# Kernel tuning notes

Measured on AMD Instinct MI355X. Metric: run time of the kernel, lower is better.

The kernel has to match this reference:

```python
import jax, jax.numpy as jnp
import numpy as np

INV_SQRT_2 = float(1.0 / np.sqrt(2.0))
INV_SQRT_3 = float(1.0 / np.sqrt(3.0))


def _silu(x):
    return x * jax.nn.sigmoid(x)


def _residual_stack(x, Ws):
    # Ws: (n_layers, 2, d, d); each layer: two (Dense -> silu), residual add, *1/sqrt(2)
    for l in range(Ws.shape[0]):
        y = x
        for i in range(Ws.shape[1]):
            y = _silu(y @ Ws[l, i])
        x = (x + y) * INV_SQRT_2
    return x


def _eff_bilinear(basis, m, id_reduce, ragged, W, n_edges, kmax):
    # basis: (T, B), m: (T, I), W: (I, B, O). Ragged rows packed into dense (E, Kmax, .)
    b2 = jnp.zeros((n_edges, kmax, basis.shape[1]), basis.dtype).at[id_reduce, ragged].set(basis)
    m2 = jnp.zeros((n_edges, kmax, m.shape[1]), m.dtype).at[id_reduce, ragged].set(m)
    sum_k = jnp.einsum('ekb,eki->ebi', b2, m2)          # (E, B, I)
    return jnp.einsum('ebi,ibo->eo', sum_k, W)          # (E, O)


def setup_inputs() -> dict:
    key = jax.random.key(0)
    N, E, K = 8000, 80000, 6
    T = E * K
    D, DR, DC, DS, DT3, DB, DQ = 128, 16, 16, 16, 64, 64, 64
    ks = jax.random.split(key, 32)
    r = lambda i, shape, s=1.0: jax.random.normal(ks[i], shape, jnp.float32) * s
    w = 0.05
    return dict(
        h=r(0, (N, D)), m_st=r(1, (E, D)),
        rbf_h=jax.random.uniform(ks[2], (E, DR)),
        rbf3=jax.random.uniform(ks[3], (E, DR)),
        cbf3=jax.random.uniform(ks[4], (T, DC)),
        sbf4=jax.random.uniform(ks[5], (T, DS)),
        idx_s=jax.random.randint(ks[6], (E,), 0, N),
        idx_t=jax.random.randint(ks[7], (E,), 0, N),
        idx_swap=jax.random.permutation(ks[8], E),
        id3_kt=jax.random.randint(ks[9], (T,), 0, E),
        id3_st=jnp.repeat(jnp.arange(E), K),
        id3_ragged_idx=jnp.tile(jnp.arange(K), E),
        edge_nb_idx=jnp.repeat(jnp.arange(E), K),
        edge_nb_ragged_idx=jnp.tile(jnp.arange(K), E),
        Kt=K, Kq=K,
        W_skip=r(10, (D, D), w),
        Wt_mkt=r(11, (D, D), w), Wt_rbf=r(12, (DR, D), w), Wt_down=r(13, (D, DT3), w),
        Wt_cbf=r(14, (DT3, DC, DB), w), Wt_up_st=r(15, (DB, D), w), Wt_up_ts=r(16, (DB, D), w),
        Wq_down=r(17, (D, DQ), w), Wq_sbf=r(18, (DQ, DS, DQ), w),
        Wq_up_st=r(19, (DQ, D), w), Wq_up_ts=r(20, (DQ, D), w),
        Wres_before=r(21, (1, 2, D, D), w), Wres_after=r(22, (2, 2, D, D), w),
        Wres_m=r(23, (1, 2, D, D), w),
        W_ae_rbf=r(24, (DR, D), w), W_ae_dense=r(25, (D, D), w), W_ae_res=r(26, (2, 2, D, D), w),
        W_asi=r(27, (3 * D, D), w),
    )


def reference(h, m_st, rbf_h, rbf3, cbf3, sbf4, idx_s, idx_t, idx_swap, id3_kt,
              id3_st, id3_ragged_idx, edge_nb_idx, edge_nb_ragged_idx, Kt, Kq,
              W_skip, Wt_mkt, Wt_rbf, Wt_down, Wt_cbf, Wt_up_st, Wt_up_ts,
              Wq_down, Wq_sbf, Wq_up_st, Wq_up_ts, Wres_before, Wres_after,
              Wres_m, W_ae_rbf, W_ae_dense, W_ae_res, W_asi):
    N, E = h.shape[0], m_st.shape[0]

    x_skip = m_st @ W_skip

    # Quadruplet interaction (ScaleFactor == identity)
    m_d = _silu(m_st @ Wq_down)                       # (E, emb_quad)
    m_nb = m_d[edge_nb_idx]                            # (E_NB, emb_quad)
    xq = _eff_bilinear(sbf4, m_nb, edge_nb_idx, edge_nb_ragged_idx, Wq_sbf, E, Kq)
    x4 = (_silu(xq @ Wq_up_st) + _silu(xq @ Wq_up_ts)[idx_swap]) * INV_SQRT_2

    # Triplet interaction
    m_kt = _silu(m_st @ Wt_mkt)
    m_kt = m_kt * (rbf3 @ Wt_rbf)                      # scale_rbf identity
    m_kt = _silu(m_kt @ Wt_down)                       # (E, emb_triplet)
    m_kt = m_kt[id3_kt]                                # (T, emb_triplet)
    xt = _eff_bilinear(cbf3, m_kt, id3_st, id3_ragged_idx, Wt_cbf, E, Kt)
    x3 = (_silu(xt @ Wt_up_st) + _silu(xt @ Wt_up_ts)[idx_swap]) * INV_SQRT_2

    x = (x_skip + x3 + x4) * INV_SQRT_3
    x = _residual_stack(x, Wres_before)
    m = (m_st + x) * INV_SQRT_2
    m = _residual_stack(m, Wres_after)

    # AtomEmbedding: rbf-gated scatter-add of edge messages to target atoms
    x_ae = m * (rbf_h @ W_ae_rbf)
    h2 = jax.ops.segment_sum(x_ae, idx_t, num_segments=N)   # scale_sum identity
    h2 = _silu(h2 @ W_ae_dense)
    h2 = _residual_stack(h2, W_ae_res)
    h_new = (h + h2) * INV_SQRT_2

    # AtomSelfInteraction
    m2 = _silu(jnp.concatenate([h_new[idx_s], h_new[idx_t], m], axis=-1) @ W_asi)
    m2 = _residual_stack(m2, Wres_m)
    m_out = (m + m2) * INV_SQRT_2
    return h_new, m_out
```

## Files before the change

kernel.cpp:

```cpp
#include <hip/hip_runtime.h>

#define INV_SQRT_2 0.70710678118654752440f
#define INV_SQRT_3 0.57735026918962576451f

typedef __bf16 bf16_t;
typedef __bf16 bf16x8 __attribute__((ext_vector_type(8)));
typedef __bf16 bf16x4 __attribute__((ext_vector_type(4)));
typedef float f32x4 __attribute__((ext_vector_type(4)));

__device__ __forceinline__ float toF(float x) { return x; }
__device__ __forceinline__ float toF(bf16_t x) { return (float)x; }
__device__ __forceinline__ float siluf(float x) { return x / (1.f + __expf(-x)); }

__device__ __forceinline__ bf16x8 ld8(const bf16_t* p) { return *(const bf16x8*)p; }
__device__ __forceinline__ bf16x8 ld8(const float* p) {
  bf16x8 r;
#pragma unroll
  for (int j = 0; j < 8; ++j) r[j] = (bf16_t)p[j];
  return r;
}

__device__ __forceinline__ float ldsc(const void* p, int f32, size_t i) {
  return f32 ? ((const float*)p)[i] : toF(((const bf16_t*)p)[i]);
}

__device__ __forceinline__ f32x4 MFMA(bf16x8 a, bf16x8 b, f32x4 c) {
  return __builtin_amdgcn_mfma_f32_16x16x32_bf16(a, b, c, 0, 0, 0);
}

__device__ __forceinline__ void zero8(f32x4 (&a)[8]) {
#pragma unroll
  for (int i = 0; i < 8; ++i)
#pragma unroll
    for (int q = 0; q < 4; ++q) a[i][q] = 0.f;
}
__device__ __forceinline__ void zero4(f32x4 (&a)[4]) {
#pragma unroll
  for (int i = 0; i < 4; ++i)
#pragma unroll
    for (int q = 0; q < 4; ++q) a[i][q] = 0.f;
}

__device__ __forceinline__ bf16x8 ldB(const bf16_t* Bp, int ks, int nt, int NT, int lane) {
  return *(const bf16x8*)(Bp + ((((size_t)ks * NT + nt) * 64 + lane) << 3));
}

__device__ __forceinline__ void ldA(bf16x8 (&af)[4], const void* p, int f32, size_t row, int g) {
  if (f32) {
    const float* q = (const float*)p + row * 128 + (g << 3);
#pragma unroll
    for (int ks = 0; ks < 4; ++ks) af[ks] = ld8(q + ks * 32);
  } else {
    const bf16_t* q = (const bf16_t*)p + row * 128 + (g << 3);
#pragma unroll
    for (int ks = 0; ks < 4; ++ks) af[ks] = ld8(q + ks * 32);
  }
}

struct St8 { bf16x8 v[8]; };
__device__ __forceinline__ void issue8(St8& r, const bf16_t* src, int tid) {
#pragma unroll
  for (int i = 0; i < 8; ++i) r.v[i] = *(const bf16x8*)(src + ((i * 256 + tid) << 3));
}
__device__ __forceinline__ void commit8(const St8& r, bf16_t* dst, int tid) {
#pragma unroll
  for (int i = 0; i < 8; ++i) *(bf16x8*)&dst[(i * 256 + tid) << 3] = r.v[i];
}
struct St4 { bf16x8 v[4]; };
__device__ __forceinline__ void issue4(St4& r, const bf16_t* src, int tid) {
#pragma unroll
  for (int i = 0; i < 4; ++i) r.v[i] = *(const bf16x8*)(src + ((i * 256 + tid) << 3));
}
__device__ __forceinline__ void commit4(const St4& r, bf16_t* dst, int tid) {
#pragma unroll
  for (int i = 0; i < 4; ++i) *(bf16x8*)&dst[(i * 256 + tid) << 3] = r.v[i];
}

template <int KS, int NT>
__device__ __forceinline__ void pass_glob(f32x4 (&acc)[NT], const bf16x8* af,
                                          const bf16_t* Wbuf, int lane) {
#pragma unroll
  for (int ks = 0; ks < KS; ++ks)
#pragma unroll
    for (int nt = 0; nt < NT; ++nt)
      acc[nt] = MFMA(af[ks], *(const bf16x8*)&Wbuf[((ks * NT + nt) * 64 + lane) << 3], acc[nt]);
}
template <int KS>
__device__ __forceinline__ void pass_slab(f32x4 (&acc)[8], const bf16_t* slab,
                                          const bf16_t* Wbuf, int lane) {
  const int rc = lane & 15, g = lane >> 4;
#pragma unroll
  for (int ks = 0; ks < KS; ++ks) {
    bf16x8 a = *(const bf16x8*)&slab[rc * 136 + ks * 32 + (g << 3)];
#pragma unroll
    for (int nt = 0; nt < 8; ++nt)
      acc[nt] = MFMA(a, *(const bf16x8*)&Wbuf[((ks * 8 + nt) * 64 + lane) << 3], acc[nt]);
  }
}

__global__ void k_detect(const unsigned short* __restrict__ probe, int* __restrict__ flag) {
  __shared__ int cnt;
  if (threadIdx.x == 0) cnt = 0;
  __syncthreads();
  int bad = 0;
  for (int i = threadIdx.x; i < 256; i += 64) {
    unsigned int u = (unsigned int)probe[i] << 16;
    float v = __uint_as_float(u);
    if (!(v == v) || fabsf(v) > 4.f || v < -0.25f) bad++;
  }
  atomicAdd(&cnt, bad);
  __syncthreads();
  if (threadIdx.x == 0) *flag = (cnt > 16) ? 1 : 0;
}

__global__ void k_zero(float* __restrict__ p, int n) {
  int i = blockIdx.x * blockDim.x + threadIdx.x;
  if (i < n) p[i] = 0.f;
}

struct RDesc { const void* src; int K, N, Kpad, dstoff, mode; };
struct RTable { RDesc d[25]; };

__global__ void k_repack(const int* __restrict__ flag, RTable tab, bf16_t* __restrict__ out) {
  const int ws = *flag;
  RDesc d = tab.d[blockIdx.y];
  int p = blockIdx.x * 256 + threadIdx.x;
  int sz = d.Kpad * d.N;
  if (p >= sz) return;
  const int bilin = d.mode & 1;
  const int Koff = d.mode >> 1;
  int NT = d.N >> 4;
  int j = p & 7;
  int lane = (p >> 3) & 63;
  int q = p >> 9;
  int nt = q % NT, ks = q / NT;
  int k = ks * 32 + ((lane >> 4) << 3) + j;
  int col = nt * 16 + (lane & 15);
  size_t si = bilin ? ((size_t)(k & 63) * 16 + (k >> 6)) * 64 + col
                    : (size_t)(k + Koff) * d.N + col;
  float v = (k < d.K) ? ldsc(d.src, ws, si) : 0.f;
  bf16_t hi = (bf16_t)v;
  out[d.dstoff + p] = hi;
  out[d.dstoff + sz + p] = (bf16_t)(v - (float)hi);
}

__global__ __launch_bounds__(256) void k_bil(const int* __restrict__ flag,
    const void* __restrict__ basis, const bf16_t* __restrict__ msrc,
    const int* __restrict__ gidx, const bf16_t* __restrict__ Wc,
    bf16_t* __restrict__ out) {
  const int ws = *flag;
  __shared__ __align__(16) bf16_t Ms[96 * 72];
  __shared__ __align__(16) float Bas[16 * 100];
  __shared__ __align__(16) bf16_t P[16384];
  const int tid = threadIdx.x;
  const int e0 = blockIdx.x * 16;
#pragma unroll
  for (int it = 0; it < 3; ++it) {
    int c = tid + it * 256;
    int j = c >> 3, part = c & 7;
    int row = gidx[e0 * 6 + j];
    *(bf16x8*)&Ms[j * 72 + part * 8] = ld8(msrc + (size_t)row * 64 + part * 8);
  }
#pragma unroll
  for (int it = 0; it < 6; ++it) {
    int c = tid + it * 256;
    Bas[(c / 96) * 100 + (c % 96)] = ldsc(basis, ws, (size_t)e0 * 96 + c);
  }
  __syncthreads();
  {
    const int e = tid >> 4, sub = tid & 15, i0 = sub * 4;
    float acc[16][4];
#pragma unroll
    for (int b = 0; b < 16; ++b)
#pragma unroll
      for (int j = 0; j < 4; ++j) acc[b][j] = 0.f;
#pragma unroll
    for (int k = 0; k < 6; ++k) {
      bf16x4 mv = *(const bf16x4*)&Ms[(e * 6 + k) * 72 + i0];
      float mf[4];
#pragma unroll
      for (int j = 0; j < 4; ++j) mf[j] = (float)mv[j];
      const float* bp = &Bas[e * 100 + k * 16];
#pragma unroll
      for (int b4 = 0; b4 < 4; ++b4) {
        f32x4 bv = *(const f32x4*)&bp[b4 * 4];
#pragma unroll
        for (int bb = 0; bb < 4; ++bb)
#pragma unroll
          for (int j = 0; j < 4; ++j) acc[b4 * 4 + bb][j] += bv[bb] * mf[j];
      }
    }
#pragma unroll
    for (int b = 0; b < 16; ++b) {
      int kk = b * 64 + i0;
      int ks = kk >> 5, r5 = kk & 31;
      int lane_hi = r5 >> 3, jj = r5 & 7;
      bf16x4 w;
#pragma unroll
      for (int j = 0; j < 4; ++j) w[j] = (bf16_t)acc[b][j];
      *(bf16x4*)&P[ks * 512 + lane_hi * 128 + e * 8 + jj] = w;
    }
  }
  __syncthreads();
  const int lane = tid & 63, wid = tid >> 6;
  const int rc = lane & 15, g = lane >> 4;
  f32x4 oa[4];
  zero4(oa);
  if (ws) {
#pragma unroll
    for (int k4 = 0; k4 < 8; ++k4)
#pragma unroll
      for (int j = 0; j < 4; ++j) {
        int ks = k4 * 4 + j;
        bf16x8 a = *(const bf16x8*)&P[ks * 512 + lane * 8];
        oa[j] = MFMA(a, ldB(Wc, ks, wid, 4, lane), oa[j]);
        oa[j] = MFMA(a, ldB(Wc + 65536, ks, wid, 4, lane), oa[j]);
      }
  } else {
#pragma unroll
    for (int k4 = 0; k4 < 8; ++k4)
#pragma unroll
      for (int j = 0; j < 4; ++j) {
        int ks = k4 * 4 + j;
        bf16x8 a = *(const bf16x8*)&P[ks * 512 + lane * 8];
        oa[j] = MFMA(a, ldB(Wc, ks, wid, 4, lane), oa[j]);
      }
  }
  f32x4 oacc = (oa[0] + oa[1]) + (oa[2] + oa[3]);
  bf16_t* op = out + ((size_t)e0 + g * 4) * 64 + wid * 16 + rc;
#pragma unroll
  for (int r = 0; r < 4; ++r) op[(size_t)r * 64] = (bf16_t)oacc[r];
}

__global__ __launch_bounds__(256, 2) void k_mkt2(const int* __restrict__ flag,
    const void* __restrict__ mst, const void* __restrict__ rbf3,
    const bf16_t* __restrict__ Wm, const bf16_t* __restrict__ Wr,
    bf16_t* __restrict__ out) {
  const int ws = *flag;
  __shared__ __align__(16) bf16_t Wb[2][16384];
  __shared__ __align__(16) bf16_t Wrl[8192];
  const int tid = threadIdx.x;
  const int lane = tid & 63, wid = tid >> 6;
  const int grow0 = blockIdx.x * 64 + wid * 16;
  const int rc = lane & 15, g = lane >> 4;
  St8 s8;
  issue8(s8, Wm, tid);
  bf16x8 wr[4];
#pragma unroll
  for (int i = 0; i < 4; ++i) wr[i] = *(const bf16x8*)(Wr + ((i * 256 + tid) << 3));
  commit8(s8, Wb[0], tid);
#pragma unroll
  for (int i = 0; i < 4; ++i) *(bf16x8*)&Wrl[(i * 256 + tid) << 3] = wr[i];
  __syncthreads();
  bf16x8 af[4];
  ldA(af, mst, ws, (size_t)(grow0 + rc), g);
  bf16x8 az;
#pragma unroll
  for (int j = 0; j < 8; ++j) az[j] = (bf16_t)0.f;
  if (g < 2) {
    if (ws) az = ld8((const float*)rbf3 + (size_t)(grow0 + rc) * 16 + (g << 3));
    else    az = ld8((const bf16_t*)rbf3 + (size_t)(grow0 + rc) * 16 + (g << 3));
  }
  f32x4 ag[8];
  zero8(ag);
#pragma unroll
  for (int nt = 0; nt < 8; ++nt) {
    ag[nt] = MFMA(az, *(const bf16x8*)&Wrl[(nt * 64 + lane) << 3], ag[nt]);
    if (ws) ag[nt] = MFMA(az, *(const bf16x8*)&Wrl[4096 + ((nt * 64 + lane) << 3)], ag[nt]);
  }
  f32x4 am[8];
  zero8(am);
  if (ws) issue8(s8, Wm + 16384, tid);
  pass_glob<4, 8>(am, af, Wb[0], lane);
  if (ws) {
    commit8(s8, Wb[1], tid);
    __syncthreads();
    pass_glob<4, 8>(am, af, Wb[1], lane);
  }
  bf16_t* op = out + (size_t)(grow0 + g * 4) * 128 + rc;
#pragma unroll
  for (int nt = 0; nt < 8; ++nt)
#pragma unroll
    for (int r = 0; r < 4; ++r)
      op[(size_t)r * 128 + nt * 16] = (bf16_t)(siluf(am[nt][r]) * ag[nt][r]);
}

__global__ __launch_bounds__(256, 4) void k_gemmE2(const int* __restrict__ flag, int a_rt,
    const void* __restrict__ A, const bf16_t* __restrict__ W, bf16_t* __restrict__ out) {
  const int ws = *flag;
  const int af32 = a_rt & ws;
  __shared__ __align__(16) bf16_t Wb[2][8192];
  const int tid = threadIdx.x;
  const int lane = tid & 63, wid = tid >> 6;
  const int grow0 = blockIdx.x * 64 + wid * 16;
  const int rc = lane & 15, g = lane >> 4;
  St4 s4;
  issue4(s4, W, tid);
  commit4(s4, Wb[0], tid);
  __syncthreads();
  bf16x8 af[4];
  ldA(af, A, af32, (size_t)(grow0 + rc), g);
  f32x4 acc[4];
  zero4(acc);
  if (ws) issue4(s4, W + 8192, tid);
  pass_glob<4, 4>(acc, af, Wb[0], lane);
  if (ws) {
    commit4(s4, Wb[1], tid);
    __syncthreads();
    pass_glob<4, 4>(acc, af, Wb[1], lane);
  }
  bf16_t* op = out + (size_t)(grow0 + g * 4) * 64 + rc;
#pragma unroll
  for (int nt = 0; nt < 4; ++nt)
#pragma unroll
    for (int r = 0; r < 4; ++r) op[(size_t)r * 64 + nt * 16] = (bf16_t)siluf(acc[nt][r]);
}

__global__ __launch_bounds__(256, 2) void k_gemmN2(const int* __restrict__ flag,
    const float* __restrict__ A, const bf16_t* __restrict__ W, bf16_t* __restrict__ out) {
  const int ws = *flag;
  __shared__ __align__(16) bf16_t Wb[2][16384];
  const int tid = threadIdx.x;
  const int lane = tid & 63, wid = tid >> 6;
  const int grow0 = blockIdx.x * 64 + wid * 16;
  const int rc = lane & 15, g = lane >> 4;
  St8 s8;
  issue8(s8, W, tid);
  commit8(s8, Wb[0], tid);
  __syncthreads();
  bf16x8 af[4];
  {
    const float* q = A + (size_t)(grow0 + rc) * 128 + (g << 3);
#pragma unroll
    for (int ks = 0; ks < 4; ++ks) af[ks] = ld8(q + ks * 32);
  }
  f32x4 acc[8];
  zero8(acc);
  if (ws) issue8(s8, W + 16384, tid);
  pass_glob<4, 8>(acc, af, Wb[0], lane);
  if (ws) {
    commit8(s8, Wb[1], tid);
    __syncthreads();
    pass_glob<4, 8>(acc, af, Wb[1], lane);
  }
  bf16_t* op = out + (size_t)(grow0 + g * 4) * 128 + rc;
#pragma unroll
  for (int nt = 0; nt < 8; ++nt)
#pragma unroll
    for (int r = 0; r < 4; ++r) op[(size_t)r * 128 + nt * 16] = (bf16_t)siluf(acc[nt][r]);
}

__global__ __launch_bounds__(256, 2) void k_comb2(const int* __restrict__ flag,
    const void* __restrict__ mst, const bf16_t* __restrict__ xt,
    const bf16_t* __restrict__ xq, const int* __restrict__ idx_swap,
    const bf16_t* Wsk, const bf16_t* Wtst, const bf16_t* Wtts,
    const bf16_t* Wqst, const bf16_t* Wqts, bf16_t* __restrict__ X) {
  const int ws = *flag;
  __shared__ __align__(16) bf16_t Wb[2][16384];
  const int tid = threadIdx.x;
  const int lane = tid & 63, wid = tid >> 6;
  const int grow0 = blockIdx.x * 64 + wid * 16;
  const int rc = lane & 15, g = lane >> 4;
  const int arow = grow0 + rc;
  const int srow = idx_swap[arow];
  const bf16_t* wseq[5] = {Wsk, Wtst, Wtts, Wqst, Wqts};
  const int SZs[5] = {16384, 8192, 8192, 8192, 8192};
  St8 s8;
  issue8(s8, wseq[0], tid);
  commit8(s8, Wb[0], tid);
  __syncthreads();
  int cur = 0;
  const int NP = ws ? 2 : 1;
  f32x4 total[8], acc[8];
  zero8(acc);
  bf16x8 af[4];
  for (int l = 0; l < 5; ++l) {
    if (l == 0) {
      ldA(af, mst, ws, (size_t)arow, g);
    } else {
      const bf16_t* asrc = (l <= 2) ? xt : xq;
      int r = (l == 1 || l == 3) ? arow : srow;
      af[0] = ld8(asrc + (size_t)r * 64 + (g << 3));
      af[1] = ld8(asrc + (size_t)r * 64 + 32 + (g << 3));
    }
    for (int p = 0; p < NP; ++p) {
      const bool last = (l == 4) && (p == NP - 1);
      if (!last) issue8(s8, (ws && p == 0) ? wseq[l] + SZs[l] : wseq[l + 1], tid);
      if (l == 0) pass_glob<4, 8>(acc, af, Wb[cur], lane);
      else        pass_glob<2, 8>(acc, af, Wb[cur], lane);
      if (!last) {
        commit8(s8, Wb[cur ^ 1], tid);
        __syncthreads();
        cur ^= 1;
      }
    }
    if (l == 0) {
#pragma unroll
      for (int nt = 0; nt < 8; ++nt) total[nt] = acc[nt] * INV_SQRT_3;
    } else {
#pragma unroll
      for (int nt = 0; nt < 8; ++nt)
#pragma unroll
        for (int r = 0; r < 4; ++r)
          total[nt][r] += siluf(acc[nt][r]) * (INV_SQRT_2 * INV_SQRT_3);
    }
    zero8(acc);
  }
  bf16_t* op = X + (size_t)(grow0 + g * 4) * 128 + rc;
#pragma unroll
  for (int nt = 0; nt < 8; ++nt)
#pragma unroll
    for (int r = 0; r < 4; ++r) op[(size_t)r * 128 + nt * 16] = (bf16_t)total[nt][r];
}

__global__ __launch_bounds__(256, 2) void k_resE2(const int* __restrict__ flag,
    const bf16_t* __restrict__ Xg, const void* __restrict__ mst,
    const bf16_t* W0, const bf16_t* W1, const bf16_t* W2,
    const bf16_t* W3, const bf16_t* W4, const bf16_t* W5,
    bf16_t* __restrict__ outg) {
  const int ws = *flag;
  __shared__ __align__(16) bf16_t Xs[64 * 136];
  __shared__ __align__(16) bf16_t Ys[64 * 136];
  __shared__ __align__(16) bf16_t Wb[16384];
  const int tid = threadIdx.x;
  const int lane = tid & 63, wid = tid >> 6;
  const int grow0 = blockIdx.x * 64 + wid * 16;
  const int rc = lane & 15, g = lane >> 4;
  bf16_t* slabX = Xs + wid * (16 * 136);
  bf16_t* slabY = Ys + wid * (16 * 136);
  const bf16_t* Wl[6] = {W0, W1, W2, W3, W4, W5};
  const bf16_t* seq[12];
  int NW;
  if (ws) {
    NW = 12;
#pragma unroll
    for (int l = 0; l < 6; ++l) { seq[2 * l] = Wl[l]; seq[2 * l + 1] = Wl[l] + 16384; }
  } else {
    NW = 6;
#pragma unroll
    for (int l = 0; l < 6; ++l) seq[l] = Wl[l];
  }
  St8 s8;
  issue8(s8, seq[0], tid);
#pragma unroll
  for (int i = 0; i < 4; ++i) {
    int o = (i * 64 + lane) * 8, r = o >> 7, c = o & 127;
    *(bf16x8*)&slabX[r * 136 + c] = *(const bf16x8*)&Xg[(size_t)(grow0 + r) * 128 + c];
  }
  commit8(s8, Wb, tid);
  __syncthreads();
  f32x4 acc[8];
  zero8(acc);
  for (int s = 0; s < NW; ++s) {
    if (s + 1 < NW) issue8(s8, seq[s + 1], tid);
    const int gg = ws ? (s >> 1) : s;
    const int fin = ws ? (s & 1) : 1;
    pass_slab<4>(acc, (gg & 1) ? slabY : slabX, Wb, lane);
    __syncthreads();
    if (s + 1 < NW) commit8(s8, Wb, tid);
    if (fin) {
      if ((gg & 1) == 0) {
#pragma unroll
        for (int nt = 0; nt < 8; ++nt)
#pragma unroll
          for (int r = 0; r < 4; ++r)
            slabY[(g * 4 + r) * 136 + nt * 16 + rc] = (bf16_t)siluf(acc[nt][r]);
      } else {
#pragma unroll
        for (int nt = 0; nt < 8; ++nt)
#pragma unroll
          for (int r = 0; r < 4; ++r) {
            int ix = (g * 4 + r) * 136 + nt * 16 + rc;
            float v = ((float)slabX[ix] + siluf(acc[nt][r])) * INV_SQRT_2;
            if (gg == 1)
              v = (ldsc(mst, ws, (size_t)(grow0 + g * 4 + r) * 128 + nt * 16 + rc) + v) *
                  INV_SQRT_2;
            slabX[ix] = (bf16_t)v;
          }
      }
      zero8(acc);
    }
    if (s + 1 < NW) __syncthreads();
  }
#pragma unroll
  for (int i = 0; i < 4; ++i) {
    int o = (i * 64 + lane) * 8, r = o >> 7, c = o & 127;
    *(bf16x8*)&outg[(size_t)(grow0 + r) * 128 + c] = *(const bf16x8*)&slabX[r * 136 + c];
  }
}

__global__ __launch_bounds__(256, 2) void k_resN2(const int* __restrict__ flag,
    bf16_t* __restrict__ Xg, const bf16_t* W0, const bf16_t* W1,
    const bf16_t* W2, const bf16_t* W3) {
  const int ws = *flag;
  __shared__ __align__(16) bf16_t Xs[64 * 136];
  __shared__ __align__(16) bf16_t Ys[64 * 136];
  __shared__ __align__(16) bf16_t Wb[16384];
  const int tid = threadIdx.x;
  const int lane = tid & 63, wid = tid >> 6;
  const int grow0 = blockIdx.x * 64 + wid * 16;
  const int rc = lane & 15, g = lane >> 4;
  bf16_t* slabX = Xs + wid * (16 * 136);
  bf16_t* slabY = Ys + wid * (16 * 136);
  const bf16_t* Wl[4] = {W0, W1, W2, W3};
  const bf16_t* seq[8];
  int NW;
  if (ws) {
    NW = 8;
#pragma unroll
    for (int l = 0; l < 4; ++l) { seq[2 * l] = Wl[l]; seq[2 * l + 1] = Wl[l] + 16384; }
  } else {
    NW = 4;
#pragma unroll
    for (int l = 0; l < 4; ++l) seq[l] = Wl[l];
  }
  St8 s8;
  issue8(s8, seq[0], tid);
#pragma unroll
  for (int i = 0; i < 4; ++i) {
    int o = (i * 64 + lane) * 8, r = o >> 7, c = o & 127;
    *(bf16x8*)&slabX[r * 136 + c] = *(const bf16x8*)&Xg[(size_t)(grow0 + r) * 128 + c];
  }
  commit8(s8, Wb, tid);
  __syncthreads();
  f32x4 acc[8];
  zero8(acc);
  for (int s = 0; s < NW; ++s) {
    if (s + 1 < NW) issue8(s8, seq[s + 1], tid);
    const int gg = ws ? (s >> 1) : s;
    const int fin = ws ? (s & 1) : 1;
    pass_slab<4>(acc, (gg & 1) ? slabY : slabX, Wb, lane);
    __syncthreads();
    if (s + 1 < NW) commit8(s8, Wb, tid);
    if (fin) {
      if ((gg & 1) == 0) {
#pragma unroll
        for (int nt = 0; nt < 8; ++nt)
#pragma unroll
          for (int r = 0; r < 4; ++r)
            slabY[(g * 4 + r) * 136 + nt * 16 + rc] = (bf16_t)siluf(acc[nt][r]);
      } else {
#pragma unroll
        for (int nt = 0; nt < 8; ++nt)
#pragma unroll
          for (int r = 0; r < 4; ++r) {
            int ix = (g * 4 + r) * 136 + nt * 16 + rc;
            slabX[ix] = (bf16_t)(((float)slabX[ix] + siluf(acc[nt][r])) * INV_SQRT_2);
          }
      }
      zero8(acc);
    }
    if (s + 1 < NW) __syncthreads();
  }
#pragma unroll
  for (int i = 0; i < 4; ++i) {
    int o = (i * 64 + lane) * 8, r = o >> 7, c = o & 127;
    *(bf16x8*)&Xg[(size_t)(grow0 + r) * 128 + c] = *(const bf16x8*)&slabX[r * 136 + c];
  }
}

__global__ __launch_bounds__(256, 2) void k_asi2(const int* __restrict__ flag,
    const bf16_t* __restrict__ hnew, const bf16_t* __restrict__ m,
    const int* __restrict__ idx_s, const int* __restrict__ idx_t,
    const bf16_t* Wasi, const bf16_t* Wm0, const bf16_t* Wm1,
    void* __restrict__ outm, int eoff) {
  const int ws = *flag;
  __shared__ __align__(16) bf16_t Xs[64 * 136];
  __shared__ __align__(16) bf16_t Ys[64 * 136];
  __shared__ __align__(16) bf16_t Wb[16384];
  const int tid = threadIdx.x;
  const int lane = tid & 63, wid = tid >> 6;
  const int grow0 = blockIdx.x * 64 + wid * 16;
  const int rc = lane & 15, g = lane >> 4;
  bf16_t* slabX = Xs + wid * (16 * 136);
  bf16_t* slabY = Ys + wid * (16 * 136);
  const int e = grow0 + rc;
  const int rs = idx_s[e], rt = idx_t[e];
  const bf16_t* seq[10];
  int NW;
  if (ws) {
    NW = 10;
    seq[0] = Wasi;         seq[1] = Wasi + 49152;
    seq[2] = Wasi + 16384; seq[3] = Wasi + 65536;
    seq[4] = Wasi + 32768; seq[5] = Wasi + 81920;
    seq[6] = Wm0;          seq[7] = Wm0 + 16384;
    seq[8] = Wm1;          seq[9] = Wm1 + 16384;
  } else {
    NW = 5;
    seq[0] = Wasi; seq[1] = Wasi + 16384; seq[2] = Wasi + 32768;
    seq[3] = Wm0;  seq[4] = Wm1;
  }
  St8 s8;
  issue8(s8, seq[0], tid);
  commit8(s8, Wb, tid);
  __syncthreads();
  f32x4 acc[8];
  zero8(acc);
  bf16x8 af[4];
  for (int s = 0; s < NW; ++s) {
    if (s + 1 < NW) issue8(s8, seq[s + 1], tid);
    const int lg = ws ? (s >> 1) : s;
    const int first = ws ? !(s & 1) : 1;
    const int fin = ws ? (s & 1) : 1;
    if (lg <= 2) {
      if (first) {
        const bf16_t* asrc = (lg == 0) ? hnew + (size_t)rs * 128
                           : (lg == 1) ? hnew + (size_t)rt * 128
                                       : m + (size_t)e * 128;
#pragma unroll
        for (int ks = 0; ks < 4; ++ks) af[ks] = ld8(asrc + ks * 32 + (g << 3));
      }
      pass_glob<4, 8>(acc, af, Wb, lane);
    } else if (lg == 3) {
      pass_slab<4>(acc, slabX, Wb, lane);
    } else {
      pass_slab<4>(acc, slabY, Wb, lane);
    }
    __syncthreads();
    if (s + 1 < NW) commit8(s8, Wb, tid);
    if (fin) {
      if (lg == 2) {
#pragma unroll
        for (int nt = 0; nt < 8; ++nt)
#pragma unroll
          for (int r = 0; r < 4; ++r)
            slabX[(g * 4 + r) * 136 + nt * 16 + rc] = (bf16_t)siluf(acc[nt][r]);
        zero8(acc);
      } else if (lg == 3) {
#pragma unroll
        for (int nt = 0; nt < 8; ++nt)
#pragma unroll
          for (int r = 0; r < 4; ++r)
            slabY[(g * 4 + r) * 136 + nt * 16 + rc] = (bf16_t)siluf(acc[nt][r]);
        zero8(acc);
      } else if (lg == 4) {
#pragma unroll
        for (int nt = 0; nt < 8; ++nt)
#pragma unroll
          for (int r = 0; r < 4; ++r) {
            int row = grow0 + g * 4 + r, col = nt * 16 + rc;
            float x = (float)slabX[(g * 4 + r) * 136 + col];
            float v = (x + siluf(acc[nt][r])) * INV_SQRT_2;
            float res = (toF(m[(size_t)row * 128 + col]) + v) * INV_SQRT_2;
            size_t oi = (size_t)eoff + (size_t)row * 128 + col;
            if (ws) ((float*)outm)[oi] = res;
            else    ((bf16_t*)outm)[oi] = (bf16_t)res;
          }
      }
    }
    if (s + 1 < NW) __syncthreads();
  }
}

__global__ void k_scatter(const int* __restrict__ flag, const bf16_t* __restrict__ m,
                          const void* __restrict__ rbf_h, const void* __restrict__ Wrbf,
                          const int* __restrict__ idx_t, float* __restrict__ h2) {
  const int ws = *flag;
  int e = blockIdx.x;
  int c = threadIdx.x;
  float gt = 0.f;
  if (ws) {
    const float* rh = (const float*)rbf_h + (size_t)e * 16;
    const float* w = (const float*)Wrbf;
#pragma unroll
    for (int k = 0; k < 16; ++k) gt += rh[k] * w[k * 128 + c];
  } else {
    const bf16_t* rh = (const bf16_t*)rbf_h + (size_t)e * 16;
    const bf16_t* w = (const bf16_t*)Wrbf;
#pragma unroll
    for (int k = 0; k < 16; ++k) gt += toF(rh[k]) * toF(w[k * 128 + c]);
  }
  atomicAdd(&h2[(size_t)idx_t[e] * 128 + c], toF(m[(size_t)e * 128 + c]) * gt);
}

__global__ void k_hnew(const int* __restrict__ flag, const void* __restrict__ h,
                       bf16_t* __restrict__ X, void* __restrict__ out, int n) {
  const int ws = *flag;
  int i = blockIdx.x * blockDim.x + threadIdx.x;
  if (i >= n) return;
  float v = (ldsc(h, ws, i) + toF(X[i])) * INV_SQRT_2;
  X[i] = (bf16_t)v;
  if (ws) ((float*)out)[i] = v;
  else    ((bf16_t*)out)[i] = (bf16_t)v;
}

extern "C" void kernel_launch(void* const* d_in, const int* in_sizes, int n_in,
                              void* d_out, int out_size, void* d_ws, size_t ws_size,
                              hipStream_t stream) {
  const int D = 128;
  const int N = in_sizes[0] / D;
  const int E = in_sizes[1] / D;

  char* base = (char*)d_ws;
  bf16_t* Wpack = (bf16_t*)base;
  int* flag = (int*)(base + 1916928 + 32768);
  char* dyn = base + 1916928 + 32768 + 256;
  size_t U = (size_t)E * 64 * sizeof(bf16_t);
  bf16_t* s0 = (bf16_t*)dyn;
  bf16_t* s1 = (bf16_t*)(dyn + U);
  bf16_t* s2 = (bf16_t*)(dyn + 2 * U);
  bf16_t* s3 = (bf16_t*)(dyn + 3 * U);
  float* h2 = (float*)(dyn + 2 * U);
  bf16_t* Rn2 = (bf16_t*)((char*)h2 + (size_t)N * 128 * sizeof(float));

  k_detect<<<1, 64, 0, stream>>>((const unsigned short*)d_in[2], flag);

  struct Def { int idx; int Krows; int K, Np, Kpad, bilin; };
  const Def defs[25] = {
      {23, 0, 128, 64, 128, 0},
      {17, 0, 128, 128, 128, 0},
      {18, 0, 16, 128, 32, 0},
      {19, 0, 128, 64, 128, 0},
      {21, 0, 64, 128, 64, 0},
      {22, 0, 64, 128, 64, 0},
      {25, 0, 64, 128, 64, 0},
      {26, 0, 64, 128, 64, 0},
      {16, 0, 128, 128, 128, 0},
      {27, 0, 128, 128, 128, 0},
      {27, 128, 128, 128, 128, 0},
      {28, 0, 128, 128, 128, 0},
      {28, 128, 128, 128, 128, 0},
      {28, 256, 128, 128, 128, 0},
      {28, 384, 128, 128, 128, 0},
      {29, 0, 128, 128, 128, 0},
      {29, 128, 128, 128, 128, 0},
      {31, 0, 128, 128, 128, 0},
      {32, 0, 128, 128, 128, 0},
      {32, 128, 128, 128, 128, 0},
      {32, 256, 128, 128, 128, 0},
      {32, 384, 128, 128, 128, 0},
      {33, 0, 384, 128, 384, 0},
      {20, 0, 1024, 64, 1024, 1},
      {24, 0, 1024, 64, 1024, 1},
  };
  RTable tab;
  int off[25];
  int cur = 0;
  for (int i = 0; i < 25; ++i) {
    off[i] = cur;
    tab.d[i].src = d_in[defs[i].idx];
    tab.d[i].K = defs[i].K;
    tab.d[i].N = defs[i].Np;
    tab.d[i].Kpad = defs[i].Kpad;
    tab.d[i].dstoff = cur;
    tab.d[i].mode = (defs[i].Krows << 1) | defs[i].bilin;
    cur += 2 * defs[i].Kpad * defs[i].Np;
  }

  k_repack<<<dim3(256, 25), 256, 0, stream>>>(flag, tab, Wpack);

  bf16_t* mkt_tmp = s0;
  bf16_t* m_kt = s2;
  bf16_t* m_d  = s3;
  bf16_t* xt = s0;
  bf16_t* xq = s1;
  bf16_t* X  = s2;
  bf16_t* R2 = s0;

  const int gE64 = E / 64;
  const int gN64 = N / 64;

  k_mkt2<<<gE64, 256, 0, stream>>>(flag, d_in[1], d_in[3], Wpack + off[1], Wpack + off[2],
                                   mkt_tmp);
  k_gemmE2<<<gE64, 256, 0, stream>>>(flag, 0, mkt_tmp, Wpack + off[3], m_kt);
  k_gemmE2<<<gE64, 256, 0, stream>>>(flag, 1, d_in[1], Wpack + off[0], m_d);
  k_bil<<<E / 16, 256, 0, stream>>>(flag, d_in[4], m_kt, (const int*)d_in[9], Wpack + off[23],
                                    xt);
  k_bil<<<E / 16, 256, 0, stream>>>(flag, d_in[5], m_d, (const int*)d_in[12], Wpack + off[24],
                                    xq);
  k_comb2<<<gE64, 256, 0, stream>>>(flag, d_in[1], xt, xq, (const int*)d_in[8],
      Wpack + off[8], Wpack + off[4], Wpack + off[5], Wpack + off[6], Wpack + off[7], X);
  k_resE2<<<gE64, 256, 0, stream>>>(flag, X, d_in[1], Wpack + off[9], Wpack + off[10],
      Wpack + off[11], Wpack + off[12], Wpack + off[13], Wpack + off[14], R2);
  k_zero<<<(N * 128 + 255) / 256, 256, 0, stream>>>(h2, N * 128);
  k_scatter<<<E, 128, 0, stream>>>(flag, R2, d_in[2], d_in[30], (const int*)d_in[7], h2);
  k_gemmN2<<<gN64, 256, 0, stream>>>(flag, h2, Wpack + off[17], Rn2);
  k_resN2<<<gN64, 256, 0, stream>>>(flag, Rn2, Wpack + off[18], Wpack + off[19],
                                    Wpack + off[20], Wpack + off[21]);
  k_hnew<<<(N * 128 + 255) / 256, 256, 0, stream>>>(flag, d_in[0], Rn2, d_out, N * 128);
  k_asi2<<<gE64, 256, 0, stream>>>(flag, Rn2, R2, (const int*)d_in[6], (const int*)d_in[7],
      Wpack + off[22], Wpack + off[15], Wpack + off[16], d_out, N * 128);
}
```

Baseline: 741.5 us.

## Widen GEMM blocks to 512 threads and double-buffer weight tiles in residual kernels

Several edge and node GEMM kernels now use 512-thread blocks covering 128 rows, so each staged weight tile in shared memory serves twice as many rows and fewer blocks reload weights. The residual and self-interaction kernels switch from a single weight buffer with two barriers per step to a double buffer with one barrier, letting the next weight load overlap compute. Node kernels gain row bounds guards for the partial last block, and silu uses a hardware reciprocal instead of a division. In exchange, shared memory per block roughly doubles, which lowers occupancy (launch bounds drop to one block per CU for the residual kernels) and reduces the number of blocks across the device.

```diff
diff --git a/kernel.cpp b/kernel.cpp
--- a/kernel.cpp
+++ b/kernel.cpp
@@ -10,7 +10,9 @@
 
 __device__ __forceinline__ float toF(float x) { return x; }
 __device__ __forceinline__ float toF(bf16_t x) { return (float)x; }
-__device__ __forceinline__ float siluf(float x) { return x / (1.f + __expf(-x)); }
+__device__ __forceinline__ float siluf(float x) {
+  return x * __builtin_amdgcn_rcpf(1.f + __expf(-x));
+}
 
 __device__ __forceinline__ bf16x8 ld8(const bf16_t* p) { return *(const bf16x8*)p; }
 __device__ __forceinline__ bf16x8 ld8(const float* p) {
@@ -57,21 +59,21 @@
   }
 }
 
-struct St8 { bf16x8 v[8]; };
-__device__ __forceinline__ void issue8(St8& r, const bf16_t* src, int tid) {
-#pragma unroll
-  for (int i = 0; i < 8; ++i) r.v[i] = *(const bf16x8*)(src + ((i * 256 + tid) << 3));
-}
-__device__ __forceinline__ void commit8(const St8& r, bf16_t* dst, int tid) {
-#pragma unroll
-  for (int i = 0; i < 8; ++i) *(bf16x8*)&dst[(i * 256 + tid) << 3] = r.v[i];
+struct Sw4 { bf16x8 v[4]; };
+__device__ __forceinline__ void issue512(Sw4& r, const bf16_t* src, int tid) {
+#pragma unroll
+  for (int i = 0; i < 4; ++i) r.v[i] = *(const bf16x8*)(src + ((i * 512 + tid) << 3));
+}
+__device__ __forceinline__ void commit512(const Sw4& r, bf16_t* dst, int tid) {
+#pragma unroll
+  for (int i = 0; i < 4; ++i) *(bf16x8*)&dst[(i * 512 + tid) << 3] = r.v[i];
 }
 struct St4 { bf16x8 v[4]; };
-__device__ __forceinline__ void issue4(St4& r, const bf16_t* src, int tid) {
+__device__ __forceinline__ void issue256(St4& r, const bf16_t* src, int tid) {
 #pragma unroll
   for (int i = 0; i < 4; ++i) r.v[i] = *(const bf16x8*)(src + ((i * 256 + tid) << 3));
 }
-__device__ __forceinline__ void commit4(const St4& r, bf16_t* dst, int tid) {
+__device__ __forceinline__ void commit256(const St4& r, bf16_t* dst, int tid) {
 #pragma unroll
   for (int i = 0; i < 4; ++i) *(bf16x8*)&dst[(i * 256 + tid) << 3] = r.v[i];
 }
@@ -232,7 +234,7 @@
   for (int r = 0; r < 4; ++r) op[(size_t)r * 64] = (bf16_t)oacc[r];
 }
 
-__global__ __launch_bounds__(256, 2) void k_mkt2(const int* __restrict__ flag,
+__global__ __launch_bounds__(512, 2) void k_mkt2(const int* __restrict__ flag,
     const void* __restrict__ mst, const void* __restrict__ rbf3,
     const bf16_t* __restrict__ Wm, const bf16_t* __restrict__ Wr,
     bf16_t* __restrict__ out) {
@@ -241,16 +243,15 @@
   __shared__ __align__(16) bf16_t Wrl[8192];
   const int tid = threadIdx.x;
   const int lane = tid & 63, wid = tid >> 6;
-  const int grow0 = blockIdx.x * 64 + wid * 16;
+  const int grow0 = blockIdx.x * 128 + wid * 16;
   const int rc = lane & 15, g = lane >> 4;
-  St8 s8;
-  issue8(s8, Wm, tid);
-  bf16x8 wr[4];
-#pragma unroll
-  for (int i = 0; i < 4; ++i) wr[i] = *(const bf16x8*)(Wr + ((i * 256 + tid) << 3));
-  commit8(s8, Wb[0], tid);
-#pragma unroll
-  for (int i = 0; i < 4; ++i) *(bf16x8*)&Wrl[(i * 256 + tid) << 3] = wr[i];
+  Sw4 s4;
+  issue512(s4, Wm, tid);
+  bf16x8 wr0 = *(const bf16x8*)(Wr + (tid << 3));
+  bf16x8 wr1 = *(const bf16x8*)(Wr + 4096 + (tid << 3));
+  commit512(s4, Wb[0], tid);
+  *(bf16x8*)&Wrl[tid << 3] = wr0;
+  *(bf16x8*)&Wrl[4096 + (tid << 3)] = wr1;
   __syncthreads();
   bf16x8 af[4];
   ldA(af, mst, ws, (size_t)(grow0 + rc), g);
@@ -270,10 +271,10 @@
   }
   f32x4 am[8];
   zero8(am);
-  if (ws) issue8(s8, Wm + 16384, tid);
+  if (ws) issue512(s4, Wm + 16384, tid);
   pass_glob<4, 8>(am, af, Wb[0], lane);
   if (ws) {
-    commit8(s8, Wb[1], tid);
+    commit512(s4, Wb[1], tid);
     __syncthreads();
     pass_glob<4, 8>(am, af, Wb[1], lane);
   }
@@ -295,17 +296,17 @@
   const int grow0 = blockIdx.x * 64 + wid * 16;
   const int rc = lane & 15, g = lane >> 4;
   St4 s4;
-  issue4(s4, W, tid);
-  commit4(s4, Wb[0], tid);
+  issue256(s4, W, tid);
+  commit256(s4, Wb[0], tid);
   __syncthreads();
   bf16x8 af[4];
   ldA(af, A, af32, (size_t)(grow0 + rc), g);
   f32x4 acc[4];
   zero4(acc);
-  if (ws) issue4(s4, W + 8192, tid);
+  if (ws) issue256(s4, W + 8192, tid);
   pass_glob<4, 4>(acc, af, Wb[0], lane);
   if (ws) {
-    commit4(s4, Wb[1], tid);
+    commit256(s4, Wb[1], tid);
     __syncthreads();
     pass_glob<4, 4>(acc, af, Wb[1], lane);
   }
@@ -316,41 +317,50 @@
     for (int r = 0; r < 4; ++r) op[(size_t)r * 64 + nt * 16] = (bf16_t)siluf(acc[nt][r]);
 }
 
-__global__ __launch_bounds__(256, 2) void k_gemmN2(const int* __restrict__ flag,
-    const float* __restrict__ A, const bf16_t* __restrict__ W, bf16_t* __restrict__ out) {
+__global__ __launch_bounds__(512, 2) void k_gemmN2(const int* __restrict__ flag,
+    const float* __restrict__ A, const bf16_t* __restrict__ W, bf16_t* __restrict__ out,
+    int M) {
   const int ws = *flag;
   __shared__ __align__(16) bf16_t Wb[2][16384];
   const int tid = threadIdx.x;
   const int lane = tid & 63, wid = tid >> 6;
-  const int grow0 = blockIdx.x * 64 + wid * 16;
+  const int grow0 = blockIdx.x * 128 + wid * 16;
+  const bool act = grow0 < M;
   const int rc = lane & 15, g = lane >> 4;
-  St8 s8;
-  issue8(s8, W, tid);
-  commit8(s8, Wb[0], tid);
+  Sw4 s4;
+  issue512(s4, W, tid);
+  commit512(s4, Wb[0], tid);
   __syncthreads();
   bf16x8 af[4];
-  {
+  if (act) {
     const float* q = A + (size_t)(grow0 + rc) * 128 + (g << 3);
 #pragma unroll
     for (int ks = 0; ks < 4; ++ks) af[ks] = ld8(q + ks * 32);
+  } else {
+#pragma unroll
+    for (int ks = 0; ks < 4; ++ks)
+#pragma unroll
+      for (int j = 0; j < 8; ++j) af[ks][j] = (bf16_t)0.f;
   }
   f32x4 acc[8];
   zero8(acc);
-  if (ws) issue8(s8, W + 16384, tid);
+  if (ws) issue512(s4, W + 16384, tid);
   pass_glob<4, 8>(acc, af, Wb[0], lane);
   if (ws) {
-    commit8(s8, Wb[1], tid);
+    commit512(s4, Wb[1], tid);
     __syncthreads();
     pass_glob<4, 8>(acc, af, Wb[1], lane);
   }
-  bf16_t* op = out + (size_t)(grow0 + g * 4) * 128 + rc;
-#pragma unroll
-  for (int nt = 0; nt < 8; ++nt)
-#pragma unroll
-    for (int r = 0; r < 4; ++r) op[(size_t)r * 128 + nt * 16] = (bf16_t)siluf(acc[nt][r]);
-}
-
-__global__ __launch_bounds__(256, 2) void k_comb2(const int* __restrict__ flag,
+  if (act) {
+    bf16_t* op = out + (size_t)(grow0 + g * 4) * 128 + rc;
+#pragma unroll
+    for (int nt = 0; nt < 8; ++nt)
+#pragma unroll
+      for (int r = 0; r < 4; ++r) op[(size_t)r * 128 + nt * 16] = (bf16_t)siluf(acc[nt][r]);
+  }
+}
+
+__global__ __launch_bounds__(512, 2) void k_comb2(const int* __restrict__ flag,
     const void* __restrict__ mst, const bf16_t* __restrict__ xt,
     const bf16_t* __restrict__ xq, const int* __restrict__ idx_swap,
     const bf16_t* Wsk, const bf16_t* Wtst, const bf16_t* Wtts,
@@ -359,15 +369,15 @@
   __shared__ __align__(16) bf16_t Wb[2][16384];
   const int tid = threadIdx.x;
   const int lane = tid & 63, wid = tid >> 6;
-  const int grow0 = blockIdx.x * 64 + wid * 16;
+  const int grow0 = blockIdx.x * 128 + wid * 16;
   const int rc = lane & 15, g = lane >> 4;
   const int arow = grow0 + rc;
   const int srow = idx_swap[arow];
   const bf16_t* wseq[5] = {Wsk, Wtst, Wtts, Wqst, Wqts};
   const int SZs[5] = {16384, 8192, 8192, 8192, 8192};
-  St8 s8;
-  issue8(s8, wseq[0], tid);
-  commit8(s8, Wb[0], tid);
+  Sw4 s4;
+  issue512(s4, wseq[0], tid);
+  commit512(s4, Wb[0], tid);
   __syncthreads();
   int cur = 0;
   const int NP = ws ? 2 : 1;
@@ -385,11 +395,11 @@
     }
     for (int p = 0; p < NP; ++p) {
       const bool last = (l == 4) && (p == NP - 1);
-      if (!last) issue8(s8, (ws && p == 0) ? wseq[l] + SZs[l] : wseq[l + 1], tid);
+      if (!last) issue512(s4, (ws && p == 0) ? wseq[l] + SZs[l] : wseq[l + 1], tid);
       if (l == 0) pass_glob<4, 8>(acc, af, Wb[cur], lane);
       else        pass_glob<2, 8>(acc, af, Wb[cur], lane);
       if (!last) {
-        commit8(s8, Wb[cur ^ 1], tid);
+        commit512(s4, Wb[cur ^ 1], tid);
         __syncthreads();
         cur ^= 1;
       }
@@ -413,18 +423,18 @@
     for (int r = 0; r < 4; ++r) op[(size_t)r * 128 + nt * 16] = (bf16_t)total[nt][r];
 }
 
-__global__ __launch_bounds__(256, 2) void k_resE2(const int* __restrict__ flag,
+__global__ __launch_bounds__(512, 1) void k_resE2(const int* __restrict__ flag,
     const bf16_t* __restrict__ Xg, const void* __restrict__ mst,
     const bf16_t* W0, const bf16_t* W1, const bf16_t* W2,
     const bf16_t* W3, const bf16_t* W4, const bf16_t* W5,
     bf16_t* __restrict__ outg) {
   const int ws = *flag;
-  __shared__ __align__(16) bf16_t Xs[64 * 136];
-  __shared__ __align__(16) bf16_t Ys[64 * 136];
-  __shared__ __align__(16) bf16_t Wb[16384];
+  __shared__ __align__(16) bf16_t Xs[128 * 136];
+  __shared__ __align__(16) bf16_t Ys[128 * 136];
+  __shared__ __align__(16) bf16_t Wb[2][16384];
   const int tid = threadIdx.x;
   const int lane = tid & 63, wid = tid >> 6;
-  const int grow0 = blockIdx.x * 64 + wid * 16;
+  const int grow0 = blockIdx.x * 128 + wid * 16;
   const int rc = lane & 15, g = lane >> 4;
   bf16_t* slabX = Xs + wid * (16 * 136);
   bf16_t* slabY = Ys + wid * (16 * 136);
@@ -440,24 +450,23 @@
 #pragma unroll
     for (int l = 0; l < 6; ++l) seq[l] = Wl[l];
   }
-  St8 s8;
-  issue8(s8, seq[0], tid);
+  Sw4 s4;
+  issue512(s4, seq[0], tid);
 #pragma unroll
   for (int i = 0; i < 4; ++i) {
     int o = (i * 64 + lane) * 8, r = o >> 7, c = o & 127;
     *(bf16x8*)&slabX[r * 136 + c] = *(const bf16x8*)&Xg[(size_t)(grow0 + r) * 128 + c];
   }
-  commit8(s8, Wb, tid);
+  commit512(s4, Wb[0], tid);
   __syncthreads();
   f32x4 acc[8];
   zero8(acc);
+  int cur = 0;
   for (int s = 0; s < NW; ++s) {
-    if (s + 1 < NW) issue8(s8, seq[s + 1], tid);
+    if (s + 1 < NW) issue512(s4, seq[s + 1], tid);
     const int gg = ws ? (s >> 1) : s;
     const int fin = ws ? (s & 1) : 1;
-    pass_slab<4>(acc, (gg & 1) ? slabY : slabX, Wb, lane);
-    __syncthreads();
-    if (s + 1 < NW) commit8(s8, Wb, tid);
+    pass_slab<4>(acc, (gg & 1) ? slabY : slabX, Wb[cur], lane);
     if (fin) {
       if ((gg & 1) == 0) {
 #pragma unroll
@@ -480,7 +489,11 @@
       }
       zero8(acc);
     }
-    if (s + 1 < NW) __syncthreads();
+    if (s + 1 < NW) {
+      commit512(s4, Wb[cur ^ 1], tid);
+      __syncthreads();
+      cur ^= 1;
+    }
   }
 #pragma unroll
   for (int i = 0; i < 4; ++i) {
@@ -489,16 +502,17 @@
   }
 }
 
-__global__ __launch_bounds__(256, 2) void k_resN2(const int* __restrict__ flag,
+__global__ __launch_bounds__(512, 1) void k_resN2(const int* __restrict__ flag,
     bf16_t* __restrict__ Xg, const bf16_t* W0, const bf16_t* W1,
-    const bf16_t* W2, const bf16_t* W3) {
-  const int ws = *flag;
-  __shared__ __align__(16) bf16_t Xs[64 * 136];
-  __shared__ __align__(16) bf16_t Ys[64 * 136];
-  __shared__ __align__(16) bf16_t Wb[16384];
+    const bf16_t* W2, const bf16_t* W3, int M) {
+  const int ws = *flag;
+  __shared__ __align__(16) bf16_t Xs[128 * 136];
+  __shared__ __align__(16) bf16_t Ys[128 * 136];
+  __shared__ __align__(16) bf16_t Wb[2][16384];
   const int tid = threadIdx.x;
   const int lane = tid & 63, wid = tid >> 6;
-  const int grow0 = blockIdx.x * 64 + wid * 16;
+  const int grow0 = blockIdx.x * 128 + wid * 16;
+  const bool act = grow0 < M;
   const int rc = lane & 15, g = lane >> 4;
   bf16_t* slabX = Xs + wid * (16 * 136);
   bf16_t* slabY = Ys + wid * (16 * 136);
@@ -514,24 +528,25 @@
 #pragma unroll
     for (int l = 0; l < 4; ++l) seq[l] = Wl[l];
   }
-  St8 s8;
-  issue8(s8, seq[0], tid);
-#pragma unroll
-  for (int i = 0; i < 4; ++i) {
-    int o = (i * 64 + lane) * 8, r = o >> 7, c = o & 127;
-    *(bf16x8*)&slabX[r * 136 + c] = *(const bf16x8*)&Xg[(size_t)(grow0 + r) * 128 + c];
-  }
-  commit8(s8, Wb, tid);
+  Sw4 s4;
+  issue512(s4, seq[0], tid);
+  if (act) {
+#pragma unroll
+    for (int i = 0; i < 4; ++i) {
+      int o = (i * 64 + lane) * 8, r = o >> 7, c = o & 127;
+      *(bf16x8*)&slabX[r * 136 + c] = *(const bf16x8*)&Xg[(size_t)(grow0 + r) * 128 + c];
+    }
+  }
+  commit512(s4, Wb[0], tid);
   __syncthreads();
   f32x4 acc[8];
   zero8(acc);
+  int cur = 0;
   for (int s = 0; s < NW; ++s) {
-    if (s + 1 < NW) issue8(s8, seq[s + 1], tid);
+    if (s + 1 < NW) issue512(s4, seq[s + 1], tid);
     const int gg = ws ? (s >> 1) : s;
     const int fin = ws ? (s & 1) : 1;
-    pass_slab<4>(acc, (gg & 1) ? slabY : slabX, Wb, lane);
-    __syncthreads();
-    if (s + 1 < NW) commit8(s8, Wb, tid);
+    pass_slab<4>(acc, (gg & 1) ? slabY : slabX, Wb[cur], lane);
     if (fin) {
       if ((gg & 1) == 0) {
 #pragma unroll
@@ -550,27 +565,33 @@
       }
       zero8(acc);
     }
-    if (s + 1 < NW) __syncthreads();
-  }
-#pragma unroll
-  for (int i = 0; i < 4; ++i) {
-    int o = (i * 64 + lane) * 8, r = o >> 7, c = o & 127;
-    *(bf16x8*)&Xg[(size_t)(grow0 + r) * 128 + c] = *(const bf16x8*)&slabX[r * 136 + c];
-  }
-}
-
-__global__ __launch_bounds__(256, 2) void k_asi2(const int* __restrict__ flag,
+    if (s + 1 < NW) {
+      commit512(s4, Wb[cur ^ 1], tid);
+      __syncthreads();
+      cur ^= 1;
+    }
+  }
+  if (act) {
+#pragma unroll
+    for (int i = 0; i < 4; ++i) {
+      int o = (i * 64 + lane) * 8, r = o >> 7, c = o & 127;
+      *(bf16x8*)&Xg[(size_t)(grow0 + r) * 128 + c] = *(const bf16x8*)&slabX[r * 136 + c];
+    }
+  }
+}
+
+__global__ __launch_bounds__(512, 1) void k_asi2(const int* __restrict__ flag,
     const bf16_t* __restrict__ hnew, const bf16_t* __restrict__ m,
     const int* __restrict__ idx_s, const int* __restrict__ idx_t,
     const bf16_t* Wasi, const bf16_t* Wm0, const bf16_t* Wm1,
     void* __restrict__ outm, int eoff) {
   const int ws = *flag;
-  __shared__ __align__(16) bf16_t Xs[64 * 136];
-  __shared__ __align__(16) bf16_t Ys[64 * 136];
-  __shared__ __align__(16) bf16_t Wb[16384];
+  __shared__ __align__(16) bf16_t Xs[128 * 136];
+  __shared__ __align__(16) bf16_t Ys[128 * 136];
+  __shared__ __align__(16) bf16_t Wb[2][16384];
   const int tid = threadIdx.x;
   const int lane = tid & 63, wid = tid >> 6;
-  const int grow0 = blockIdx.x * 64 + wid * 16;
+  const int grow0 = blockIdx.x * 128 + wid * 16;
   const int rc = lane & 15, g = lane >> 4;
   bf16_t* slabX = Xs + wid * (16 * 136);
   bf16_t* slabY = Ys + wid * (16 * 136);
@@ -590,15 +611,16 @@
     seq[0] = Wasi; seq[1] = Wasi + 16384; seq[2] = Wasi + 32768;
     seq[3] = Wm0;  seq[4] = Wm1;
   }
-  St8 s8;
-  issue8(s8, seq[0], tid);
-  commit8(s8, Wb, tid);
+  Sw4 s4;
+  issue512(s4, seq[0], tid);
+  commit512(s4, Wb[0], tid);
   __syncthreads();
   f32x4 acc[8];
   zero8(acc);
   bf16x8 af[4];
+  int cur = 0;
   for (int s = 0; s < NW; ++s) {
-    if (s + 1 < NW) issue8(s8, seq[s + 1], tid);
+    if (s + 1 < NW) issue512(s4, seq[s + 1], tid);
     const int lg = ws ? (s >> 1) : s;
     const int first = ws ? !(s & 1) : 1;
     const int fin = ws ? (s & 1) : 1;
@@ -610,14 +632,12 @@
 #pragma unroll
         for (int ks = 0; ks < 4; ++ks) af[ks] = ld8(asrc + ks * 32 + (g << 3));
       }
-      pass_glob<4, 8>(acc, af, Wb, lane);
+      pass_glob<4, 8>(acc, af, Wb[cur], lane);
     } else if (lg == 3) {
-      pass_slab<4>(acc, slabX, Wb, lane);
+      pass_slab<4>(acc, slabX, Wb[cur], lane);
     } else {
-      pass_slab<4>(acc, slabY, Wb, lane);
-    }
-    __syncthreads();
-    if (s + 1 < NW) commit8(s8, Wb, tid);
+      pass_slab<4>(acc, slabY, Wb[cur], lane);
+    }
     if (fin) {
       if (lg == 2) {
 #pragma unroll
@@ -648,7 +668,11 @@
           }
       }
     }
-    if (s + 1 < NW) __syncthreads();
+    if (s + 1 < NW) {
+      commit512(s4, Wb[cur ^ 1], tid);
+      __syncthreads();
+      cur ^= 1;
+    }
   }
 }
 
@@ -757,27 +781,28 @@
   bf16_t* X  = s2;
   bf16_t* R2 = s0;
 
-  const int gE64 = E / 64;
-  const int gN64 = N / 64;
-
-  k_mkt2<<<gE64, 256, 0, stream>>>(flag, d_in[1], d_in[3], Wpack + off[1], Wpack + off[2],
-                                   mkt_tmp);
+  const int gE128 = E / 128;
+  const int gE64  = E / 64;
+  const int gN128 = (N + 127) / 128;
+
+  k_mkt2<<<gE128, 512, 0, stream>>>(flag, d_in[1], d_in[3], Wpack + off[1], Wpack + off[2],
+                                    mkt_tmp);
   k_gemmE2<<<gE64, 256, 0, stream>>>(flag, 0, mkt_tmp, Wpack + off[3], m_kt);
   k_gemmE2<<<gE64, 256, 0, stream>>>(flag, 1, d_in[1], Wpack + off[0], m_d);
   k_bil<<<E / 16, 256, 0, stream>>>(flag, d_in[4], m_kt, (const int*)d_in[9], Wpack + off[23],
                                     xt);
   k_bil<<<E / 16, 256, 0, stream>>>(flag, d_in[5], m_d, (const int*)d_in[12], Wpack + off[24],
                                     xq);
-  k_comb2<<<gE64, 256, 0, stream>>>(flag, d_in[1], xt, xq, (const int*)d_in[8],
+  k_comb2<<<gE128, 512, 0, stream>>>(flag, d_in[1], xt, xq, (const int*)d_in[8],
       Wpack + off[8], Wpack + off[4], Wpack + off[5], Wpack + off[6], Wpack + off[7], X);
-  k_resE2<<<gE64, 256, 0, stream>>>(flag, X, d_in[1], Wpack + off[9], Wpack + off[10],
+  k_resE2<<<gE128, 512, 0, stream>>>(flag, X, d_in[1], Wpack + off[9], Wpack + off[10],
       Wpack + off[11], Wpack + off[12], Wpack + off[13], Wpack + off[14], R2);
   k_zero<<<(N * 128 + 255) / 256, 256, 0, stream>>>(h2, N * 128);
   k_scatter<<<E, 128, 0, stream>>>(flag, R2, d_in[2], d_in[30], (const int*)d_in[7], h2);
-  k_gemmN2<<<gN64, 256, 0, stream>>>(flag, h2, Wpack + off[17], Rn2);
-  k_resN2<<<gN64, 256, 0, stream>>>(flag, Rn2, Wpack + off[18], Wpack + off[19],
-                                    Wpack + off[20], Wpack + off[21]);
+  k_gemmN2<<<gN128, 512, 0, stream>>>(flag, h2, Wpack + off[17], Rn2, N);
+  k_resN2<<<gN128, 512, 0, stream>>>(flag, Rn2, Wpack + off[18], Wpack + off[19],
+                                     Wpack + off[20], Wpack + off[21], N);
   k_hnew<<<(N * 128 + 255) / 256, 256, 0, stream>>>(flag, d_in[0], Rn2, d_out, N * 128);
-  k_asi2<<<gE64, 256, 0, stream>>>(flag, Rn2, R2, (const int*)d_in[6], (const int*)d_in[7],
+  k_asi2<<<gE128, 512, 0, stream>>>(flag, Rn2, R2, (const int*)d_in[6], (const int*)d_in[7],
       Wpack + off[22], Wpack + off[15], Wpack + off[16], d_out, N * 128);
 }
```

Measured after the change: 685.5 us. -7.5%, faster.
